# Kernel tuning notes

Hardware: AMD Instinct MI355X
Metric: run time of the kernel (lower is better)

The kernel has to match this reference:

```python
import jax, jax.numpy as jnp
import numpy as np

N, L, D = 100000, 4, 64          # nodes, gcn layers, emb_dim
B, S = 16384, 32                 # links, intersection-set size
INP, RELD, NREL, NDIST = 32, 32, 200, 11
PSD = L * D                      # param_set_dim = 256


def setup_inputs() -> dict:
    key = jax.random.key(0)
    ks = jax.random.split(key, 16)
    return {
        "node_repr": jax.random.normal(ks[0], (N, L, D), jnp.float32),
        "node_feat": jax.random.normal(ks[1], (N, INP), jnp.float32),
        "head_idx": jax.random.randint(ks[2], (B,), 0, N, jnp.int32),
        "rel_idx": jax.random.randint(ks[3], (B,), 0, NREL, jnp.int32),
        "tail_idx": jax.random.randint(ks[4], (B,), 0, N, jnp.int32),
        "dist": jax.random.randint(ks[5], (B,), 0, NDIST, jnp.int32),
        "inter_count": jax.random.randint(ks[6], (B, S), 0, N, jnp.int32),
        "rel_emb": jax.random.normal(ks[7], (NREL, RELD), jnp.float32),
        "dist_emb": jax.random.normal(ks[8], (NDIST, D), jnp.float32),
        "head_W": jax.random.normal(ks[9], (PSD + D, INP), jnp.float32) * 0.05,
        "head_b": jnp.zeros((INP,), jnp.float32),
        "tail_W": jax.random.normal(ks[10], (PSD + D, INP), jnp.float32) * 0.05,
        "tail_b": jnp.zeros((INP,), jnp.float32),
        "W1": jax.random.normal(ks[11], (2 * PSD + RELD + 2 * INP + PSD, 64), jnp.float32) * 0.05,
        "b1": jnp.zeros((64,), jnp.float32),
        "W2": jax.random.normal(ks[12], (64, 32), jnp.float32) * 0.05,
        "b2": jnp.zeros((32,), jnp.float32),
        "W3": jax.random.normal(ks[13], (32, 1), jnp.float32) * 0.05,
        "b3": jnp.zeros((1,), jnp.float32),
    }


def reference(node_repr, node_feat, head_idx, rel_idx, tail_idx, dist, inter_count,
              rel_emb, dist_emb, head_W, head_b, tail_W, tail_b,
              W1, b1, W2, b2, W3, b3):
    flat = node_repr.reshape(node_repr.shape[0], -1)           # [N, PSD]
    head_repr = flat[head_idx]                                 # [B, PSD]
    tail_repr = flat[tail_idx]                                 # [B, PSD]
    rel_repr = rel_emb[rel_idx]                                # [B, RELD]

    # masked gather + mean over the intersection set (-1 entries masked out)
    sign = jnp.sign(inter_count + 1).astype(flat.dtype)        # [B, S]
    mid = flat[jnp.abs(inter_count)] * sign[:, :, None]        # [B, S, PSD]
    mid = mid.sum(axis=1)                                      # [B, PSD]
    cnt = jnp.clip(jnp.sum(inter_count != -1, axis=1), 1, None)
    mid_repr = mid / cnt[:, None].astype(flat.dtype)

    dist_repr = dist_emb[dist]                                 # [B, D]

    md = jnp.concatenate([mid_repr, dist_repr], axis=1)        # [B, PSD+D]
    head_pred = md @ head_W + head_b                           # [B, INP]
    tail_pred = md @ tail_W + tail_b
    head_init_feat = node_feat[head_idx]
    tail_init_feat = node_feat[tail_idx]

    g_rep = jnp.concatenate(
        [head_repr, tail_repr, rel_repr, mid_repr, head_init_feat, tail_init_feat], axis=1)
    h = jax.nn.relu(g_rep @ W1 + b1)
    h = jax.nn.relu(h @ W2 + b2)
    output = h @ W3 + b3                                       # [B, 1]
    return (output, head_pred, tail_pred, head_init_feat, tail_init_feat)
```

## Files before the change

kernel.cpp:

```cpp
#include <hip/hip_runtime.h>
#include <cstddef>
#include <cstdint>

typedef __bf16 bf16x8 __attribute__((ext_vector_type(8)));
typedef float  f32x4  __attribute__((ext_vector_type(4)));

#define NLINK 8
#define X_STRIDE 936
#define H1_STRIDE 66
#define WTC_ELEMS (128 * 928)
#define WTC_BYTES (WTC_ELEMS * 2)

__device__ __forceinline__ float b2f(unsigned short u) {
    unsigned int x = (unsigned int)u << 16;
    return __builtin_bit_cast(float, x);
}
__device__ __forceinline__ unsigned short f2b(float f) {
    unsigned int u = __builtin_bit_cast(unsigned int, f);
    u += 0x7FFFu + ((u >> 16) & 1u);
    return (unsigned short)(u >> 16);
}

__global__ void prep_weights(const float* __restrict__ W1,
                             const float* __restrict__ headW,
                             const float* __restrict__ tailW,
                             unsigned short* __restrict__ WTc) {
    const int n = blockIdx.x;
    for (int k = threadIdx.x; k < 928; k += blockDim.x) {
        float v = 0.f;
        if (n < 64) {
            if (k < 864) v = W1[(size_t)k * 64 + n];
        } else {
            const int c = (n < 96) ? (n - 64) : (n - 96);
            const float* W = (n < 96) ? headW : tailW;
            if (k >= 544 && k < 800)      v = W[(size_t)(k - 544) * 32 + c];
            else if (k >= 864 && k < 928) v = W[(size_t)(256 + (k - 864)) * 32 + c];
        }
        WTc[(size_t)n * 928 + k] = f2b(v);
    }
}

__device__ __forceinline__ bf16x8 gather_Bfrag(const float* __restrict__ W1,
                                               const float* __restrict__ hW,
                                               const float* __restrict__ tW,
                                               int n, int k0) {
    unsigned short r[8];
    if (n < 64) {
        #pragma unroll
        for (int j = 0; j < 8; ++j) {
            const int k = k0 + j;
            r[j] = (k < 864) ? f2b(W1[(size_t)k * 64 + n]) : (unsigned short)0;
        }
    } else {
        const float* W = (n < 96) ? hW : tW;
        const int c = (n < 96) ? (n - 64) : (n - 96);
        #pragma unroll
        for (int j = 0; j < 8; ++j) {
            const int k = k0 + j;
            float v = 0.f;
            if (k >= 544 && k < 800)      v = W[(size_t)(k - 544) * 32 + c];
            else if (k >= 864 && k < 928) v = W[(size_t)(256 + (k - 864)) * 32 + c];
            r[j] = f2b(v);
        }
    }
    unsigned short tmp[8];
    #pragma unroll
    for (int j = 0; j < 8; ++j) tmp[j] = r[j];
    return __builtin_bit_cast(bf16x8, *(const uint4*)tmp);
}

template <bool USE_WTC>
__global__ __launch_bounds__(256, 6) void fused_main(
    const float* __restrict__ node_repr,
    const float* __restrict__ node_feat,
    const int* __restrict__ head_idx,
    const int* __restrict__ rel_idx,
    const int* __restrict__ tail_idx,
    const int* __restrict__ dist,
    const int* __restrict__ inter,
    const float* __restrict__ rel_emb,
    const float* __restrict__ dist_emb,
    const float* __restrict__ b1p,
    const float* __restrict__ head_bp,
    const float* __restrict__ tail_bp,
    const float* __restrict__ W2p,
    const float* __restrict__ b2p,
    const float* __restrict__ W3p,
    const float* __restrict__ b3p,
    const unsigned short* __restrict__ WTc,
    const float* __restrict__ W1p,
    const float* __restrict__ headWp,
    const float* __restrict__ tailWp,
    float* __restrict__ out,
    int B)
{
    extern __shared__ char smem[];
    unsigned short* sX  = (unsigned short*)smem;
    unsigned short* sH1 = (unsigned short*)(smem + NLINK * X_STRIDE * 2);

    const int tid  = threadIdx.x;
    const int w    = tid >> 6;
    const int lane = tid & 63;
    const int g0   = blockIdx.x * NLINK;

    float* out0   = out;
    float* out_hp = out + B;
    float* out_tp = out + B + (size_t)B * 32;
    float* out_hf = out + B + (size_t)B * 64;
    float* out_tf = out + B + (size_t)B * 96;

    for (int li = 0; li < 2; ++li) {
        const int L = w * 2 + li;
        const int g = g0 + L;
        if (g >= B) continue;

        const int hidx = head_idx[g];
        const int tidx = tail_idx[g];
        const int ridx = rel_idx[g];
        const int didx = dist[g];
        const int c4 = lane * 4;

        float4 hr = *(const float4*)(node_repr + (size_t)hidx * 256 + c4);
        float4 tr = *(const float4*)(node_repr + (size_t)tidx * 256 + c4);
        ushort4 hb; hb.x = f2b(hr.x); hb.y = f2b(hr.y); hb.z = f2b(hr.z); hb.w = f2b(hr.w);
        ushort4 tb; tb.x = f2b(tr.x); tb.y = f2b(tr.y); tb.z = f2b(tr.z); tb.w = f2b(tr.w);
        *(ushort4*)(sX + (size_t)L * X_STRIDE + c4)       = hb;
        *(ushort4*)(sX + (size_t)L * X_STRIDE + 256 + c4) = tb;

        float a0 = 0.f, a1 = 0.f, a2 = 0.f, a3 = 0.f;
        int cnt = 0;
        const int* icp = inter + (size_t)g * 32;
        #pragma unroll
        for (int s = 0; s < 32; ++s) {
            const int ic = icp[s];
            const int idx = (ic >= 0) ? ic : -ic;
            const float sg = (ic == -1) ? 0.f : ((ic >= 0) ? 1.f : -1.f);
            float4 v = *(const float4*)(node_repr + (size_t)idx * 256 + c4);
            a0 += sg * v.x; a1 += sg * v.y;
            a2 += sg * v.z; a3 += sg * v.w;
            cnt += (ic != -1) ? 1 : 0;
        }
        const float inv = 1.0f / (float)(cnt > 0 ? cnt : 1);
        ushort4 mv;
        mv.x = f2b(a0 * inv); mv.y = f2b(a1 * inv);
        mv.z = f2b(a2 * inv); mv.w = f2b(a3 * inv);
        *(ushort4*)(sX + (size_t)L * X_STRIDE + 544 + c4) = mv;

        if (lane < 32) {
            const float hf = node_feat[(size_t)hidx * 32 + lane];
            const float tf = node_feat[(size_t)tidx * 32 + lane];
            const float rv = rel_emb[(size_t)ridx * 32 + lane];
            sX[(size_t)L * X_STRIDE + 800 + lane] = f2b(hf);
            sX[(size_t)L * X_STRIDE + 832 + lane] = f2b(tf);
            sX[(size_t)L * X_STRIDE + 512 + lane] = f2b(rv);
            out_hf[(size_t)g * 32 + lane] = hf;
            out_tf[(size_t)g * 32 + lane] = tf;
        }
        sX[(size_t)L * X_STRIDE + 864 + lane] = f2b(dist_emb[(size_t)didx * 64 + lane]);
    }
    __syncthreads();

    const int col16 = lane & 15;
    const int row8  = lane & 7;
    const int quad  = lane >> 4;
    const int n0    = w * 32;

    f32x4 accv[2] = {{0.f,0.f,0.f,0.f},{0.f,0.f,0.f,0.f}};

    const unsigned short* aP = sX + (size_t)row8 * X_STRIDE + quad * 8;

    if (USE_WTC) {
        const unsigned short* bP0 = WTc + (size_t)(n0 +  0 + col16) * 928 + quad * 8;
        const unsigned short* bP1 = WTc + (size_t)(n0 + 16 + col16) * 928 + quad * 8;
        for (int ks = 0; ks < 29; ++ks) {
            const bf16x8 af = __builtin_bit_cast(bf16x8, *(const uint4*)(aP + ks * 32));
            bf16x8 b0 = __builtin_bit_cast(bf16x8, *(const uint4*)(bP0 + ks * 32));
            bf16x8 b1 = __builtin_bit_cast(bf16x8, *(const uint4*)(bP1 + ks * 32));
            accv[0] = __builtin_amdgcn_mfma_f32_16x16x32_bf16(af, b0, accv[0], 0, 0, 0);
            accv[1] = __builtin_amdgcn_mfma_f32_16x16x32_bf16(af, b1, accv[1], 0, 0, 0);
        }
    } else {
        for (int ks = 0; ks < 29; ++ks) {
            const int k0 = ks * 32 + quad * 8;
            const bf16x8 af = __builtin_bit_cast(bf16x8, *(const uint4*)(aP + ks * 32));
            bf16x8 b0 = gather_Bfrag(W1p, headWp, tailWp, n0 +  0 + col16, k0);
            bf16x8 b1 = gather_Bfrag(W1p, headWp, tailWp, n0 + 16 + col16, k0);
            accv[0] = __builtin_amdgcn_mfma_f32_16x16x32_bf16(af, b0, accv[0], 0, 0, 0);
            accv[1] = __builtin_amdgcn_mfma_f32_16x16x32_bf16(af, b1, accv[1], 0, 0, 0);
        }
    }

    if (n0 < 64) {
        #pragma unroll
        for (int t = 0; t < 2; ++t) {
            const int n = n0 + t * 16 + col16;
            const float bias = b1p[n];
            #pragma unroll
            for (int r = 0; r < 4; ++r) {
                const int row = quad * 4 + r;
                if (row < NLINK) {
                    float v = accv[t][r] + bias;
                    v = v > 0.f ? v : 0.f;
                    sH1[(size_t)row * H1_STRIDE + n] = f2b(v);
                }
            }
        }
    } else {
        const bool isH = (n0 < 96);
        const float* bp = isH ? head_bp : tail_bp;
        float* dst = isH ? out_hp : out_tp;
        #pragma unroll
        for (int t = 0; t < 2; ++t) {
            const int c = (n0 - (isH ? 64 : 96)) + t * 16 + col16;
            const float bias = bp[c];
            #pragma unroll
            for (int r = 0; r < 4; ++r) {
                const int row = quad * 4 + r;
                const int m = g0 + row;
                if (row < NLINK && m < B) dst[(size_t)m * 32 + c] = accv[t][r] + bias;
            }
        }
    }
    __syncthreads();

    const int half = lane >> 5;
    const int c    = lane & 31;
    const float w3v = W3p[c];
    const float b2v = b2p[c];
    const float b3v = b3p[0];
    {
        const int L = w * 2 + half;
        float acc = 0.f;
        #pragma unroll 8
        for (int k = 0; k < 64; ++k)
            acc += b2f(sH1[(size_t)L * H1_STRIDE + k]) * W2p[(size_t)k * 32 + c];
        const float h2 = fmaxf(acc + b2v, 0.f);
        float p = h2 * w3v;
        p += __shfl_xor(p, 16);
        p += __shfl_xor(p, 8);
        p += __shfl_xor(p, 4);
        p += __shfl_xor(p, 2);
        p += __shfl_xor(p, 1);
        if (c == 0 && (g0 + L) < B) out0[g0 + L] = p + b3v;
    }
}

extern "C" void kernel_launch(void* const* d_in, const int* in_sizes, int n_in,
                              void* d_out, int out_size, void* d_ws, size_t ws_size,
                              hipStream_t stream) {
    const float* node_repr = (const float*)d_in[0];
    const float* node_feat = (const float*)d_in[1];
    const int* head_idx = (const int*)d_in[2];
    const int* rel_idx  = (const int*)d_in[3];
    const int* tail_idx = (const int*)d_in[4];
    const int* dist     = (const int*)d_in[5];
    const int* inter    = (const int*)d_in[6];
    const float* rel_emb  = (const float*)d_in[7];
    const float* dist_emb = (const float*)d_in[8];
    const float* head_W   = (const float*)d_in[9];
    const float* head_b   = (const float*)d_in[10];
    const float* tail_W   = (const float*)d_in[11];
    const float* tail_b   = (const float*)d_in[12];
    const float* W1       = (const float*)d_in[13];
    const float* b1       = (const float*)d_in[14];
    const float* W2       = (const float*)d_in[15];
    const float* b2       = (const float*)d_in[16];
    const float* W3       = (const float*)d_in[17];
    const float* b3       = (const float*)d_in[18];

    const int B = in_sizes[2];
    float* out = (float*)d_out;

    const int grid = (B + NLINK - 1) / NLINK;
    const size_t lds = (size_t)NLINK * X_STRIDE * 2 + (size_t)NLINK * H1_STRIDE * 2;

    if (ws_size >= (size_t)WTC_BYTES) {
        unsigned short* WTc = (unsigned short*)d_ws;
        hipLaunchKernelGGL(prep_weights, dim3(128), dim3(256), 0, stream,
                           W1, head_W, tail_W, WTc);
        hipLaunchKernelGGL((fused_main<true>), dim3(grid), dim3(256), lds, stream,
                           node_repr, node_feat, head_idx, rel_idx, tail_idx, dist, inter,
                           rel_emb, dist_emb, b1, head_b, tail_b, W2, b2, W3, b3,
                           WTc, W1, head_W, tail_W, out, B);
    } else {
        hipLaunchKernelGGL((fused_main<false>), dim3(grid), dim3(256), lds, stream,
                           node_repr, node_feat, head_idx, rel_idx, tail_idx, dist, inter,
                           rel_emb, dist_emb, b1, head_b, tail_b, W2, b2, W3, b3,
                           (const unsigned short*)nullptr, W1, head_W, tail_W, out, B);
    }
}
```

Baseline: 266.7 us.

## Convert node table to bf16 shadow copy before gathering

```diff
diff --git a/kernel.cpp b/kernel.cpp
--- a/kernel.cpp
+++ b/kernel.cpp
@@ -10,6 +10,7 @@
 #define H1_STRIDE 66
 #define WTC_ELEMS (128 * 928)
 #define WTC_BYTES (WTC_ELEMS * 2)
+#define SHADOW_OFF 262144
 
 __device__ __forceinline__ float b2f(unsigned short u) {
     unsigned int x = (unsigned int)u << 16;
@@ -40,6 +41,18 @@
     }
 }
 
+__global__ __launch_bounds__(256) void conv_table(const float* __restrict__ src,
+                                                  unsigned short* __restrict__ dst,
+                                                  long n4) {
+    const long stride = (long)gridDim.x * blockDim.x;
+    for (long i = (long)blockIdx.x * blockDim.x + threadIdx.x; i < n4; i += stride) {
+        float4 v = ((const float4*)src)[i];
+        ushort4 o;
+        o.x = f2b(v.x); o.y = f2b(v.y); o.z = f2b(v.z); o.w = f2b(v.w);
+        ((ushort4*)dst)[i] = o;
+    }
+}
+
 __device__ __forceinline__ bf16x8 gather_Bfrag(const float* __restrict__ W1,
                                                const float* __restrict__ hW,
                                                const float* __restrict__ tW,
@@ -69,8 +82,8 @@
     return __builtin_bit_cast(bf16x8, *(const uint4*)tmp);
 }
 
-template <bool USE_WTC>
-__global__ __launch_bounds__(256, 6) void fused_main(
+template <int MODE>
+__global__ __launch_bounds__(256, 4) void fused_main(
     const float* __restrict__ node_repr,
     const float* __restrict__ node_feat,
     const int* __restrict__ head_idx,
@@ -88,6 +101,7 @@
     const float* __restrict__ W3p,
     const float* __restrict__ b3p,
     const unsigned short* __restrict__ WTc,
+    const unsigned short* __restrict__ shadow,
     const float* __restrict__ W1p,
     const float* __restrict__ headWp,
     const float* __restrict__ tailWp,
@@ -119,27 +133,47 @@
         const int ridx = rel_idx[g];
         const int didx = dist[g];
         const int c4 = lane * 4;
-
-        float4 hr = *(const float4*)(node_repr + (size_t)hidx * 256 + c4);
-        float4 tr = *(const float4*)(node_repr + (size_t)tidx * 256 + c4);
-        ushort4 hb; hb.x = f2b(hr.x); hb.y = f2b(hr.y); hb.z = f2b(hr.z); hb.w = f2b(hr.w);
-        ushort4 tb; tb.x = f2b(tr.x); tb.y = f2b(tr.y); tb.z = f2b(tr.z); tb.w = f2b(tr.w);
-        *(ushort4*)(sX + (size_t)L * X_STRIDE + c4)       = hb;
-        *(ushort4*)(sX + (size_t)L * X_STRIDE + 256 + c4) = tb;
+        const int* icp = inter + (size_t)g * 32;
 
         float a0 = 0.f, a1 = 0.f, a2 = 0.f, a3 = 0.f;
         int cnt = 0;
-        const int* icp = inter + (size_t)g * 32;
-        #pragma unroll
-        for (int s = 0; s < 32; ++s) {
-            const int ic = icp[s];
-            const int idx = (ic >= 0) ? ic : -ic;
-            const float sg = (ic == -1) ? 0.f : ((ic >= 0) ? 1.f : -1.f);
-            float4 v = *(const float4*)(node_repr + (size_t)idx * 256 + c4);
-            a0 += sg * v.x; a1 += sg * v.y;
-            a2 += sg * v.z; a3 += sg * v.w;
-            cnt += (ic != -1) ? 1 : 0;
-        }
+
+        if (MODE == 2) {
+            ushort4 hb = *(const ushort4*)(shadow + (size_t)hidx * 256 + c4);
+            ushort4 tb = *(const ushort4*)(shadow + (size_t)tidx * 256 + c4);
+            *(ushort4*)(sX + (size_t)L * X_STRIDE + c4)       = hb;
+            *(ushort4*)(sX + (size_t)L * X_STRIDE + 256 + c4) = tb;
+
+            #pragma unroll
+            for (int s = 0; s < 32; ++s) {
+                const int ic = icp[s];
+                const int idx = (ic >= 0) ? ic : -ic;
+                const float sg = (ic == -1) ? 0.f : ((ic >= 0) ? 1.f : -1.f);
+                ushort4 v = *(const ushort4*)(shadow + (size_t)idx * 256 + c4);
+                a0 += sg * b2f(v.x); a1 += sg * b2f(v.y);
+                a2 += sg * b2f(v.z); a3 += sg * b2f(v.w);
+                cnt += (ic != -1) ? 1 : 0;
+            }
+        } else {
+            float4 hr = *(const float4*)(node_repr + (size_t)hidx * 256 + c4);
+            float4 tr = *(const float4*)(node_repr + (size_t)tidx * 256 + c4);
+            ushort4 hb; hb.x = f2b(hr.x); hb.y = f2b(hr.y); hb.z = f2b(hr.z); hb.w = f2b(hr.w);
+            ushort4 tb; tb.x = f2b(tr.x); tb.y = f2b(tr.y); tb.z = f2b(tr.z); tb.w = f2b(tr.w);
+            *(ushort4*)(sX + (size_t)L * X_STRIDE + c4)       = hb;
+            *(ushort4*)(sX + (size_t)L * X_STRIDE + 256 + c4) = tb;
+
+            #pragma unroll
+            for (int s = 0; s < 32; ++s) {
+                const int ic = icp[s];
+                const int idx = (ic >= 0) ? ic : -ic;
+                const float sg = (ic == -1) ? 0.f : ((ic >= 0) ? 1.f : -1.f);
+                float4 v = *(const float4*)(node_repr + (size_t)idx * 256 + c4);
+                a0 += sg * v.x; a1 += sg * v.y;
+                a2 += sg * v.z; a3 += sg * v.w;
+                cnt += (ic != -1) ? 1 : 0;
+            }
+        }
+
         const float inv = 1.0f / (float)(cnt > 0 ? cnt : 1);
         ushort4 mv;
         mv.x = f2b(a0 * inv); mv.y = f2b(a1 * inv);
@@ -169,7 +203,7 @@
 
     const unsigned short* aP = sX + (size_t)row8 * X_STRIDE + quad * 8;
 
-    if (USE_WTC) {
+    if (MODE >= 1) {
         const unsigned short* bP0 = WTc + (size_t)(n0 +  0 + col16) * 928 + quad * 8;
         const unsigned short* bP1 = WTc + (size_t)(n0 + 16 + col16) * 928 + quad * 8;
         for (int ks = 0; ks < 29; ++ks) {
@@ -269,23 +303,39 @@
     const float* b3       = (const float*)d_in[18];
 
     const int B = in_sizes[2];
+    const long nrepr = in_sizes[0];
     float* out = (float*)d_out;
 
     const int grid = (B + NLINK - 1) / NLINK;
     const size_t lds = (size_t)NLINK * X_STRIDE * 2 + (size_t)NLINK * H1_STRIDE * 2;
 
-    if (ws_size >= (size_t)WTC_BYTES) {
+    const size_t shadow_bytes = (size_t)nrepr * 2;
+    const size_t need2 = (size_t)SHADOW_OFF + shadow_bytes;
+
+    if (ws_size >= need2) {
+        unsigned short* WTc    = (unsigned short*)d_ws;
+        unsigned short* shadow = (unsigned short*)((char*)d_ws + SHADOW_OFF);
+        hipLaunchKernelGGL(prep_weights, dim3(128), dim3(256), 0, stream,
+                           W1, head_W, tail_W, WTc);
+        hipLaunchKernelGGL(conv_table, dim3(2048), dim3(256), 0, stream,
+                           node_repr, shadow, nrepr / 4);
+        hipLaunchKernelGGL((fused_main<2>), dim3(grid), dim3(256), lds, stream,
+                           node_repr, node_feat, head_idx, rel_idx, tail_idx, dist, inter,
+                           rel_emb, dist_emb, b1, head_b, tail_b, W2, b2, W3, b3,
+                           WTc, shadow, W1, head_W, tail_W, out, B);
+    } else if (ws_size >= (size_t)WTC_BYTES) {
         unsigned short* WTc = (unsigned short*)d_ws;
         hipLaunchKernelGGL(prep_weights, dim3(128), dim3(256), 0, stream,
                            W1, head_W, tail_W, WTc);
-        hipLaunchKernelGGL((fused_main<true>), dim3(grid), dim3(256), lds, stream,
+        hipLaunchKernelGGL((fused_main<1>), dim3(grid), dim3(256), lds, stream,
                            node_repr, node_feat, head_idx, rel_idx, tail_idx, dist, inter,
                            rel_emb, dist_emb, b1, head_b, tail_b, W2, b2, W3, b3,
-                           WTc, W1, head_W, tail_W, out, B);
+                           WTc, (const unsigned short*)nullptr, W1, head_W, tail_W, out, B);
     } else {
-        hipLaunchKernelGGL((fused_main<false>), dim3(grid), dim3(256), lds, stream,
+        hipLaunchKernelGGL((fused_main<0>), dim3(grid), dim3(256), lds, stream,
                            node_repr, node_feat, head_idx, rel_idx, tail_idx, dist, inter,
                            rel_emb, dist_emb, b1, head_b, tail_b, W2, b2, W3, b3,
-                           (const unsigned short*)nullptr, W1, head_W, tail_W, out, B);
-    }
-}
+                           (const unsigned short*)nullptr, (const unsigned short*)nullptr,
+                           W1, head_W, tail_W, out, B);
+    }
+}
```

Result: slower. 273.5 us (+2.5%).
